# Kernel optimization log

Hardware: AMD Instinct MI355X
Metric: run time of the kernel (lower is better)

The kernel has to match this reference:

```python
import jax, jax.numpy as jnp
import numpy as np
import math

FACTOR = 5


def setup_inputs() -> dict:
    key = jax.random.key(0)
    k1, k2, k3, k4 = jax.random.split(key, 4)
    B, L, H, D = 4, 2048, 8, 64
    sample_k = FACTOR * int(np.ceil(np.log(L)))  # 40
    queries = jax.random.normal(k1, (B, L, H, D), dtype=jnp.float32)
    keys = jax.random.normal(k2, (B, L, H, D), dtype=jnp.float32)
    values = jax.random.normal(k3, (B, L, H, D), dtype=jnp.float32)
    # per-query sampled key indices (replaces the host-side random.sample loop)
    index_sample = jax.random.randint(k4, (L, sample_k), 0, L, dtype=jnp.int64)
    return {"queries": queries, "keys": keys, "values": values,
            "index_sample": index_sample}


def reference(queries, keys, values, index_sample):
    B, L_Q, H, D = queries.shape
    L_K = keys.shape[1]
    # [B, L, H, D] -> [B, H, L, D]
    Q = jnp.transpose(queries, (0, 2, 1, 3))
    K = jnp.transpose(keys, (0, 2, 1, 3))
    V = jnp.transpose(values, (0, 2, 1, 3))

    u = min(FACTOR * int(np.ceil(np.log(L_Q))), L_Q)  # n_top

    # --- _prob_QK: sample-score-topk-gather ---
    # K_sample[b,h,i,s,e] = K[b,h,index_sample[i,s],e]  -> [B,H,L_Q,S,E]
    K_sample = K[:, :, index_sample, :]
    Q_K_sample = jnp.einsum('bhie,bhise->bhis', Q, K_sample)  # [B,H,L_Q,S]
    M = Q_K_sample.max(axis=-1) - Q_K_sample.sum(axis=-1) / L_K  # [B,H,L_Q]
    _, M_top = jax.lax.top_k(M, u)  # [B,H,u] indices of sparse queries

    Q_reduce = jnp.take_along_axis(Q, M_top[..., None], axis=2)  # [B,H,u,D]
    scores = jnp.einsum('bhue,bhke->bhuk', Q_reduce, K)  # [B,H,u,L_K]

    scale = 1.0 / math.sqrt(D)
    scores = scores * scale

    # --- initial context (mask_flag=True): causal running sum of V ---
    context = jnp.cumsum(V, axis=2)  # [B,H,L_Q,D]

    # --- ProbMask: causal mask rows gathered at M_top ---
    causal_mask = jnp.arange(L_K)[None, None, None, :] > M_top[..., None]
    scores = jnp.where(causal_mask, -jnp.inf, scores)
    attn = jax.nn.softmax(scores, axis=-1)  # [B,H,u,L_K]

    update = jnp.einsum('bhuk,bhkd->bhud', attn, V)  # [B,H,u,D]
    bi = jnp.arange(B)[:, None, None]
    hi = jnp.arange(H)[None, :, None]
    context = context.at[bi, hi, M_top].set(update)

    # back to [B, L, H, D]
    return jnp.transpose(context, (0, 2, 1, 3))
```

## Files before the change

kernel.cpp:

```cpp
#include <hip/hip_runtime.h>
#include <hip/hip_bf16.h>
#include <math.h>


#define BB 4
#define LL 2048
#define HH 8
#define DD 64
#define SS 40
#define UU 40
#define CC 64
#define LC (LL/CC)

#define KC    64
#define NCH2  8
#define UG    2
#define KSUB  4
#define KPAD  68
#define PPAD  68

__global__ void k_measure(const float* __restrict__ Q, const float* __restrict__ K,
                          const int* __restrict__ idx, float* __restrict__ M)
{
    __shared__ float sMax[4][8];
    __shared__ float sSum[4][8];

    int t   = threadIdx.x;
    int blk = blockIdx.x;
    int b   = blk >> 11;
    int i   = blk & (LL - 1);
    int w    = t >> 6, lane = t & 63;
    int hg   = lane >> 4;
    int d4   = lane & 15;

    const int*   ip   = idx + (size_t)i * SS + w * 10;
    const float* Kb   = K + (size_t)b * (LL * HH * DD);
    const float* Qrow = Q + ((size_t)b * LL + i) * (HH * DD);

    float4 qa = *(const float4*)(Qrow + hg * DD + d4 * 4);
    float4 qb = *(const float4*)(Qrow + (4 + hg) * DD + d4 * 4);

    float maxa = -INFINITY, suma = 0.f;
    float maxb = -INFINITY, sumb = 0.f;

#define DOT4(q_, k_) (fmaf((q_).w, (k_).w, fmaf((q_).z, (k_).z, \
                      fmaf((q_).y, (k_).y, (q_).x * (k_).x))))

    float4 A0, B0, A1, B1;
    float4 A2, B2, A3, B3;
    {
        int k0 = ip[0], k1 = ip[1];
        const float* r0 = Kb + (size_t)k0 * (HH * DD);
        const float* r1 = Kb + (size_t)k1 * (HH * DD);
        A0 = *(const float4*)(r0 + hg * DD + d4 * 4);
        B0 = *(const float4*)(r0 + (4 + hg) * DD + d4 * 4);
        A1 = *(const float4*)(r1 + hg * DD + d4 * 4);
        B1 = *(const float4*)(r1 + (4 + hg) * DD + d4 * 4);
    }

    #pragma unroll
    for (int g = 0; g < 5; ++g) {
        if (g < 4) {
            int k2 = ip[2 * g + 2], k3 = ip[2 * g + 3];
            const float* r2 = Kb + (size_t)k2 * (HH * DD);
            const float* r3 = Kb + (size_t)k3 * (HH * DD);
            A2 = *(const float4*)(r2 + hg * DD + d4 * 4);
            B2 = *(const float4*)(r2 + (4 + hg) * DD + d4 * 4);
            A3 = *(const float4*)(r3 + hg * DD + d4 * 4);
            B3 = *(const float4*)(r3 + (4 + hg) * DD + d4 * 4);
        }
        __builtin_amdgcn_sched_barrier(0);

        float pa0 = DOT4(qa, A0), pb0 = DOT4(qb, B0);
        float pa1 = DOT4(qa, A1), pb1 = DOT4(qb, B1);
        #pragma unroll
        for (int off = 1; off < 16; off <<= 1) {
            pa0 += __shfl_xor(pa0, off);
            pb0 += __shfl_xor(pb0, off);
            pa1 += __shfl_xor(pa1, off);
            pb1 += __shfl_xor(pb1, off);
        }
        maxa = fmaxf(maxa, fmaxf(pa0, pa1));  suma += pa0 + pa1;
        maxb = fmaxf(maxb, fmaxf(pb0, pb1));  sumb += pb0 + pb1;

        A0 = A2; B0 = B2; A1 = A3; B1 = B3;
    }
#undef DOT4

    if (d4 == 0) {
        sMax[w][hg]     = maxa;  sSum[w][hg]     = suma;
        sMax[w][4 + hg] = maxb;  sSum[w][4 + hg] = sumb;
    }
    __syncthreads();

    if (t < 8) {
        float mx = sMax[0][t], sm = sSum[0][t];
        #pragma unroll
        for (int w2 = 1; w2 < 4; ++w2) {
            mx = fmaxf(mx, sMax[w2][t]);
            sm += sSum[w2][t];
        }
        M[((size_t)(b * HH + t)) * LL + i] = mx - sm * (1.0f / (float)LL);
    }
}

__global__ void k_topk(const float* __restrict__ M, int* __restrict__ topIdx)
{
    int lane = threadIdx.x;
    int bh   = blockIdx.x;
    const float* Mp = M + (size_t)bh * LL;

    unsigned k[32];
    #pragma unroll
    for (int r = 0; r < 32; ++r) {
        unsigned u = __float_as_uint(Mp[r * 64 + lane]);
        k[r] = (u & 0x80000000u) ? ~u : (u | 0x80000000u);
    }

    unsigned T = 0u;
    for (int bit = 31; bit >= 0; --bit) {
        unsigned cand = T | (1u << bit);
        int c = 0;
        #pragma unroll
        for (int r = 0; r < 32; ++r) c += (k[r] >= cand) ? 1 : 0;
        #pragma unroll
        for (int off = 1; off < 64; off <<= 1) c += __shfl_xor(c, off);
        if (c >= UU) T = cand;
    }

    int cGT = 0, cGE = 0;
    #pragma unroll
    for (int r = 0; r < 32; ++r) {
        cGT += (k[r] > T) ? 1 : 0;
        cGE += (k[r] >= T) ? 1 : 0;
    }
    #pragma unroll
    for (int off = 1; off < 64; off <<= 1) {
        cGT += __shfl_xor(cGT, off);
        cGE += __shfl_xor(cGE, off);
    }

    int need = UU - cGT;
    int X = LL;
    if (cGE - cGT != need) {
        int lo2 = 0;
        for (int bit = 10; bit >= 0; --bit) {
            int cand = lo2 | (1 << bit);
            int c = 0;
            #pragma unroll
            for (int r = 0; r < 32; ++r)
                c += (k[r] == T && (r * 64 + lane) < cand) ? 1 : 0;
            #pragma unroll
            for (int off = 1; off < 64; off <<= 1) c += __shfl_xor(c, off);
            if (c < need) lo2 = cand;
        }
        X = lo2 + 1;
    }

    unsigned inMask = 0u;
    int cnt = 0;
    #pragma unroll
    for (int r = 0; r < 32; ++r) {
        bool in = (k[r] > T) || (k[r] == T && (r * 64 + lane) < X);
        if (in) { inMask |= 1u << r; ++cnt; }
    }
    int pre = cnt;
    #pragma unroll
    for (int off = 1; off < 64; off <<= 1) {
        int v = __shfl_up(pre, off);
        if (lane >= off) pre += v;
    }
    int slot = pre - cnt;
    #pragma unroll
    for (int r = 0; r < 32; ++r) {
        if ((inMask >> r) & 1u) {
            topIdx[bh * UU + slot] = r * 64 + lane;
            ++slot;
        }
    }
}

__launch_bounds__(256, 2)
__global__ void k_attn(const float* __restrict__ Q, const float* __restrict__ K,
                       const float* __restrict__ V, const int* __restrict__ topIdx,
                       float* __restrict__ Oc, float* __restrict__ Lc)
{
    __shared__ float sK[2][KC][KPAD];
    __shared__ float sV[2][KC][KPAD];
    __shared__ float sP[20][PPAD];
    __shared__ int   sPos[UU];

    int t   = threadIdx.x;
    int bid = blockIdx.x;
    int bh  = bid / (NCH2 * UG);
    int rem = bid % (NCH2 * UG);
    int ch  = rem / UG, ug = rem % UG;
    int b   = bh / HH, h = bh % HH;

    if (t < UU) sPos[t] = topIdx[bh * UU + t];

    int j  = t & 63;
    int w  = t >> 6, lane = t & 63;
    int ub = __builtin_amdgcn_readfirstlane(w) * 5;

    int d4p = t & 15, tg = t >> 4;
    float4 a0 = {0,0,0,0}, a1 = {0,0,0,0};
    float den[5] = {0.f, 0.f, 0.f, 0.f, 0.f};

    const float* Kh = K + ((size_t)b * LL * HH + h) * DD;
    const float* Vh = V + ((size_t)b * LL * HH + h) * DD;

    float4 pk0, pk1, pk2, pk3, pv0, pv1, pv2, pv3;

#define ISSUE(k0_) { \
    size_t g0 = (size_t)((k0_) +  0 + tg) * (HH * DD) + d4p * 4; \
    size_t g1 = (size_t)((k0_) + 16 + tg) * (HH * DD) + d4p * 4; \
    size_t g2 = (size_t)((k0_) + 32 + tg) * (HH * DD) + d4p * 4; \
    size_t g3 = (size_t)((k0_) + 48 + tg) * (HH * DD) + d4p * 4; \
    pk0 = *(const float4*)(Kh + g0); pv0 = *(const float4*)(Vh + g0); \
    pk1 = *(const float4*)(Kh + g1); pv1 = *(const float4*)(Vh + g1); \
    pk2 = *(const float4*)(Kh + g2); pv2 = *(const float4*)(Vh + g2); \
    pk3 = *(const float4*)(Kh + g3); pv3 = *(const float4*)(Vh + g3); \
}
#define COMMIT(buf_) { \
    *(float4*)&sK[buf_][ 0 + tg][d4p * 4] = pk0; *(float4*)&sV[buf_][ 0 + tg][d4p * 4] = pv0; \
    *(float4*)&sK[buf_][16 + tg][d4p * 4] = pk1; *(float4*)&sV[buf_][16 + tg][d4p * 4] = pv1; \
    *(float4*)&sK[buf_][32 + tg][d4p * 4] = pk2; *(float4*)&sV[buf_][32 + tg][d4p * 4] = pv2; \
    *(float4*)&sK[buf_][48 + tg][d4p * 4] = pk3; *(float4*)&sV[buf_][48 + tg][d4p * 4] = pv3; \
}

    int k0base = ch * KSUB * KC;
    ISSUE(k0base);
    COMMIT(0);
    __syncthreads();

    #pragma unroll
    for (int sub = 0; sub < KSUB; ++sub) {
        int cur = sub & 1;
        int k0  = k0base + sub * KC;

        if (sub + 1 < KSUB) ISSUE(k0 + KC);

        int jg = k0 + j;
        {
            int p0 = __builtin_amdgcn_readfirstlane(sPos[ug * 20 + ub + 0]);
            int p1 = __builtin_amdgcn_readfirstlane(sPos[ug * 20 + ub + 1]);
            int p2 = __builtin_amdgcn_readfirstlane(sPos[ug * 20 + ub + 2]);
            int p3 = __builtin_amdgcn_readfirstlane(sPos[ug * 20 + ub + 3]);
            int p4 = __builtin_amdgcn_readfirstlane(sPos[ug * 20 + ub + 4]);
            const float* q0 = Q + (((size_t)b * LL + p0) * HH + h) * DD;
            const float* q1 = Q + (((size_t)b * LL + p1) * HH + h) * DD;
            const float* q2 = Q + (((size_t)b * LL + p2) * HH + h) * DD;
            const float* q3 = Q + (((size_t)b * LL + p3) * HH + h) * DD;
            const float* q4 = Q + (((size_t)b * LL + p4) * HH + h) * DD;
            float c0 = 0.f, c1 = 0.f, c2 = 0.f, c3 = 0.f, c4 = 0.f;
            #pragma unroll
            for (int d4 = 0; d4 < 16; ++d4) {
                float4 kk = *(const float4*)&sK[cur][j][d4 * 4];
                int d = d4 * 4;
                c0 = fmaf(kk.x, q0[d], c0); c0 = fmaf(kk.y, q0[d+1], c0);
                c0 = fmaf(kk.z, q0[d+2], c0); c0 = fmaf(kk.w, q0[d+3], c0);
                c1 = fmaf(kk.x, q1[d], c1); c1 = fmaf(kk.y, q1[d+1], c1);
                c1 = fmaf(kk.z, q1[d+2], c1); c1 = fmaf(kk.w, q1[d+3], c1);
                c2 = fmaf(kk.x, q2[d], c2); c2 = fmaf(kk.y, q2[d+1], c2);
                c2 = fmaf(kk.z, q2[d+2], c2); c2 = fmaf(kk.w, q2[d+3], c2);
                c3 = fmaf(kk.x, q3[d], c3); c3 = fmaf(kk.y, q3[d+1], c3);
                c3 = fmaf(kk.z, q3[d+2], c3); c3 = fmaf(kk.w, q3[d+3], c3);
                c4 = fmaf(kk.x, q4[d], c4); c4 = fmaf(kk.y, q4[d+1], c4);
                c4 = fmaf(kk.z, q4[d+2], c4); c4 = fmaf(kk.w, q4[d+3], c4);
            }
            float e0 = (jg > p0) ? 0.f : __expf(c0 * 0.125f);
            float e1 = (jg > p1) ? 0.f : __expf(c1 * 0.125f);
            float e2 = (jg > p2) ? 0.f : __expf(c2 * 0.125f);
            float e3 = (jg > p3) ? 0.f : __expf(c3 * 0.125f);
            float e4 = (jg > p4) ? 0.f : __expf(c4 * 0.125f);
            sP[ub + 0][j] = e0;
            sP[ub + 1][j] = e1;
            sP[ub + 2][j] = e2;
            sP[ub + 3][j] = e3;
            sP[ub + 4][j] = e4;
            #pragma unroll
            for (int off = 1; off < 64; off <<= 1) {
                e0 += __shfl_xor(e0, off);
                e1 += __shfl_xor(e1, off);
                e2 += __shfl_xor(e2, off);
                e3 += __shfl_xor(e3, off);
                e4 += __shfl_xor(e4, off);
            }
            den[0] += e0; den[1] += e1; den[2] += e2; den[3] += e3; den[4] += e4;
        }
        __syncthreads();

        if (sub + 1 < KSUB) {
            if (cur == 0) { COMMIT(1); } else { COMMIT(0); }
        }

        #pragma unroll 4
        for (int j4 = 0; j4 < KC / 4; ++j4) {
            float4 pj0 = *(const float4*)&sP[tg][j4 * 4];
            float4 pj1 = (tg < 4) ? *(const float4*)&sP[16 + tg][j4 * 4]
                                  : (float4){0,0,0,0};
            float4 va = *(const float4*)&sV[cur][j4 * 4 + 0][d4p * 4];
            float4 vb = *(const float4*)&sV[cur][j4 * 4 + 1][d4p * 4];
            float4 vc = *(const float4*)&sV[cur][j4 * 4 + 2][d4p * 4];
            float4 vd = *(const float4*)&sV[cur][j4 * 4 + 3][d4p * 4];
            a0.x = fmaf(pj0.x, va.x, fmaf(pj0.y, vb.x, fmaf(pj0.z, vc.x, fmaf(pj0.w, vd.x, a0.x))));
            a0.y = fmaf(pj0.x, va.y, fmaf(pj0.y, vb.y, fmaf(pj0.z, vc.y, fmaf(pj0.w, vd.y, a0.y))));
            a0.z = fmaf(pj0.x, va.z, fmaf(pj0.y, vb.z, fmaf(pj0.z, vc.z, fmaf(pj0.w, vd.z, a0.z))));
            a0.w = fmaf(pj0.x, va.w, fmaf(pj0.y, vb.w, fmaf(pj0.z, vc.w, fmaf(pj0.w, vd.w, a0.w))));
            a1.x = fmaf(pj1.x, va.x, fmaf(pj1.y, vb.x, fmaf(pj1.z, vc.x, fmaf(pj1.w, vd.x, a1.x))));
            a1.y = fmaf(pj1.x, va.y, fmaf(pj1.y, vb.y, fmaf(pj1.z, vc.y, fmaf(pj1.w, vd.y, a1.y))));
            a1.z = fmaf(pj1.x, va.z, fmaf(pj1.y, vb.z, fmaf(pj1.z, vc.z, fmaf(pj1.w, vd.z, a1.z))));
            a1.w = fmaf(pj1.x, va.w, fmaf(pj1.y, vb.w, fmaf(pj1.z, vc.w, fmaf(pj1.w, vd.w, a1.w))));
        }
        __syncthreads();
    }
#undef ISSUE
#undef COMMIT

    if (lane == 0) {
        int base = (bh * NCH2 + ch) * UU + ug * 20 + ub;
        Lc[base + 0] = den[0]; Lc[base + 1] = den[1]; Lc[base + 2] = den[2];
        Lc[base + 3] = den[3]; Lc[base + 4] = den[4];
    }
    {
        int u0g = ug * 20 + tg;
        size_t o0 = ((size_t)(bh * NCH2 + ch) * UU + u0g) * DD + d4p * 4;
        *(float4*)(Oc + o0) = a0;
        if (tg < 4) {
            int u1g = ug * 20 + 16 + tg;
            size_t o1 = ((size_t)(bh * NCH2 + ch) * UU + u1g) * DD + d4p * 4;
            *(float4*)(Oc + o1) = a1;
        }
    }
}

__global__ void k_chunksum(const float* __restrict__ V, float* __restrict__ chunkSum)
{
    int t  = threadIdx.x;
    int c  = blockIdx.x % CC;
    int bh = blockIdx.x / CC;
    int b  = bh / HH; int h = bh - b * HH;
    int d4 = t & 15, rs = t >> 4;

    float4 acc = {0,0,0,0};
    int l0 = c * LC;
    for (int l = l0 + rs; l < l0 + LC; l += 4) {
        float4 v = *(const float4*)(V + (((size_t)b * LL + l) * HH + h) * DD + d4 * 4);
        acc.x += v.x; acc.y += v.y; acc.z += v.z; acc.w += v.w;
    }
    acc.x += __shfl_xor(acc.x, 16); acc.y += __shfl_xor(acc.y, 16);
    acc.z += __shfl_xor(acc.z, 16); acc.w += __shfl_xor(acc.w, 16);
    acc.x += __shfl_xor(acc.x, 32); acc.y += __shfl_xor(acc.y, 32);
    acc.z += __shfl_xor(acc.z, 32); acc.w += __shfl_xor(acc.w, 32);
    if (t < 16)
        *(float4*)(chunkSum + ((size_t)bh * CC + c) * DD + d4 * 4) = acc;
}

__global__ void k_cumsum(const float* __restrict__ V, const float* __restrict__ chunkSum,
                         const float* __restrict__ Oc, const float* __restrict__ Lc,
                         const int* __restrict__ topIdx, float* __restrict__ out)
{
    int t  = threadIdx.x;
    int c  = blockIdx.x & (CC - 1);
    int bh = blockIdx.x >> 6;
    int b  = bh / HH; int h = bh - b * HH;
    int d4 = t & 15, s = t >> 4;

    const float4* CS4 = (const float4*)chunkSum;
    float4 off = {0,0,0,0};
    for (int c2 = s; c2 < c; c2 += 4) {
        float4 x = CS4[((size_t)bh * CC + c2) * 16 + d4];
        off.x += x.x; off.y += x.y; off.z += x.z; off.w += x.w;
    }
    off.x += __shfl_xor(off.x, 16); off.y += __shfl_xor(off.y, 16);
    off.z += __shfl_xor(off.z, 16); off.w += __shfl_xor(off.w, 16);
    off.x += __shfl_xor(off.x, 32); off.y += __shfl_xor(off.y, 32);
    off.z += __shfl_xor(off.z, 32); off.w += __shfl_xor(off.w, 32);

    int l0 = c * LC + s * 8;
    size_t base = (((size_t)b * LL + l0) * HH + h) * DD + d4 * 4;
    const size_t stride = (size_t)HH * DD;

    float4 v[8];
    #pragma unroll
    for (int r = 0; r < 8; ++r)
        v[r] = *(const float4*)(V + base + (size_t)r * stride);
    #pragma unroll
    for (int r = 1; r < 8; ++r) {
        v[r].x += v[r-1].x; v[r].y += v[r-1].y;
        v[r].z += v[r-1].z; v[r].w += v[r-1].w;
    }

    float4 inc = v[7];
    float4 p1;
    p1.x = __shfl_up(inc.x, 16); p1.y = __shfl_up(inc.y, 16);
    p1.z = __shfl_up(inc.z, 16); p1.w = __shfl_up(inc.w, 16);
    if (s >= 1) { inc.x += p1.x; inc.y += p1.y; inc.z += p1.z; inc.w += p1.w; }
    float4 p2;
    p2.x = __shfl_up(inc.x, 32); p2.y = __shfl_up(inc.y, 32);
    p2.z = __shfl_up(inc.z, 32); p2.w = __shfl_up(inc.w, 32);
    if (s >= 2) { inc.x += p2.x; inc.y += p2.y; inc.z += p2.z; inc.w += p2.w; }

    float4 add;
    add.x = off.x + inc.x - v[7].x;
    add.y = off.y + inc.y - v[7].y;
    add.z = off.z + inc.z - v[7].z;
    add.w = off.w + inc.w - v[7].w;

    #pragma unroll
    for (int r = 0; r < 8; ++r) {
        float4 o;
        o.x = v[r].x + add.x; o.y = v[r].y + add.y;
        o.z = v[r].z + add.z; o.w = v[r].w + add.w;
        *(float4*)(out + base + (size_t)r * stride) = o;
    }

    int l0c = c * LC;
    int anyTop = 0;
    #pragma unroll
    for (int u = 0; u < UU; ++u) {
        int pos = topIdx[bh * UU + u];
        anyTop |= (pos >= l0c && pos < l0c + LC) ? 1 : 0;
    }
    if (anyTop) {
        asm volatile("s_waitcnt vmcnt(0)" ::: "memory");
        for (int u = 0; u < UU; ++u) {
            int pos = topIdx[bh * UU + u];
            if (pos >= l0c && pos < l0c + LC) {
                float num = 0.f, den = 0.f;
                #pragma unroll
                for (int cc = 0; cc < NCH2; ++cc) {
                    num += Oc[((size_t)(bh * NCH2 + cc) * UU + u) * DD + t];
                    den += Lc[(bh * NCH2 + cc) * UU + u];
                }
                out[(((size_t)b * LL + pos) * HH + h) * DD + t] = num / den;
            }
        }
    }
}

extern "C" void kernel_launch(void* const* d_in, const int* in_sizes, int n_in,
                              void* d_out, int out_size, void* d_ws, size_t ws_size,
                              hipStream_t stream)
{
    const float* Q   = (const float*)d_in[0];
    const float* K   = (const float*)d_in[1];
    const float* V   = (const float*)d_in[2];
    const int*   idx = (const int*)d_in[3];
    float* out = (float*)d_out;

    float* M        = (float*)d_ws;
    int*   topIdx   = (int*)(M + (size_t)BB * HH * LL);
    float* Oc       = (float*)(topIdx + BB * HH * UU);
    float* Lc       = Oc + (size_t)BB * HH * NCH2 * UU * DD;
    float* chunkSum = Lc + BB * HH * NCH2 * UU;

    k_measure <<<BB * LL,             256, 0, stream>>>(Q, K, idx, M);
    k_topk    <<<BB * HH,              64, 0, stream>>>(M, topIdx);
    k_attn    <<<BB * HH * NCH2 * UG, 256, 0, stream>>>(Q, K, V, topIdx, Oc, Lc);
    k_chunksum<<<BB * HH * CC,         64, 0, stream>>>(V, chunkSum);
    k_cumsum  <<<BB * HH * CC,         64, 0, stream>>>(V, chunkSum, Oc, Lc, topIdx, out);
}
```

Measured before the change: 185.5 us.

## Merge independent stages into shared launches and add a separate finalize kernel

Folds the V chunk-sum into the measure kernel as extra blocks, and the causal cumsum into the top-k kernel as extra blocks. The top-u row overwrite moves into a small finalize kernel that runs after attention. The launch order changes so the cumsum no longer waits on attention and the cumsum path drops its per-chunk scan of topIdx. This cuts launch count and lets small independent work run alongside the larger stages, at the cost of heterogeneous blocks and a launch_bounds hint on the measure kernel.

```diff
diff --git a/kernel.cpp b/kernel.cpp
--- a/kernel.cpp
+++ b/kernel.cpp
@@ -19,14 +19,44 @@
 #define KPAD  68
 #define PPAD  68
 
-__global__ void k_measure(const float* __restrict__ Q, const float* __restrict__ K,
-                          const int* __restrict__ idx, float* __restrict__ M)
+#define NCSB  512
+#define NMSB  (BB*LL)
+#define NTKB  32
+#define NCUB  512
+
+__launch_bounds__(256, 8)
+__global__ void k_measure_cs(const float* __restrict__ Q, const float* __restrict__ K,
+                             const float* __restrict__ V, const int* __restrict__ idx,
+                             float* __restrict__ M, float* __restrict__ chunkSum)
 {
     __shared__ float sMax[4][8];
     __shared__ float sSum[4][8];
 
-    int t   = threadIdx.x;
-    int blk = blockIdx.x;
+    int t = threadIdx.x;
+
+    if (blockIdx.x < NCSB) {
+        int w = t >> 6, lane = t & 63;
+        int cI = blockIdx.x * 4 + w;
+        int bh = cI >> 6, c = cI & (CC - 1);
+        int b  = bh >> 3, h = bh & 7;
+        int d4 = lane & 15, rs = lane >> 4;
+
+        float4 acc = {0,0,0,0};
+        int l0 = c * LC;
+        for (int l = l0 + rs; l < l0 + LC; l += 4) {
+            float4 v = *(const float4*)(V + (((size_t)b * LL + l) * HH + h) * DD + d4 * 4);
+            acc.x += v.x; acc.y += v.y; acc.z += v.z; acc.w += v.w;
+        }
+        acc.x += __shfl_xor(acc.x, 16); acc.y += __shfl_xor(acc.y, 16);
+        acc.z += __shfl_xor(acc.z, 16); acc.w += __shfl_xor(acc.w, 16);
+        acc.x += __shfl_xor(acc.x, 32); acc.y += __shfl_xor(acc.y, 32);
+        acc.z += __shfl_xor(acc.z, 32); acc.w += __shfl_xor(acc.w, 32);
+        if (lane < 16)
+            *(float4*)(chunkSum + ((size_t)bh * CC + c) * DD + d4 * 4) = acc;
+        return;
+    }
+
+    int blk = blockIdx.x - NCSB;
     int b   = blk >> 11;
     int i   = blk & (LL - 1);
     int w    = t >> 6, lane = t & 63;
@@ -104,79 +134,142 @@
     }
 }
 
-__global__ void k_topk(const float* __restrict__ M, int* __restrict__ topIdx)
+__global__ void k_topk_cum(const float* __restrict__ M, int* __restrict__ topIdx,
+                           const float* __restrict__ V, const float* __restrict__ chunkSum,
+                           float* __restrict__ out)
 {
-    int lane = threadIdx.x;
-    int bh   = blockIdx.x;
-    const float* Mp = M + (size_t)bh * LL;
-
-    unsigned k[32];
-    #pragma unroll
-    for (int r = 0; r < 32; ++r) {
-        unsigned u = __float_as_uint(Mp[r * 64 + lane]);
-        k[r] = (u & 0x80000000u) ? ~u : (u | 0x80000000u);
-    }
-
-    unsigned T = 0u;
-    for (int bit = 31; bit >= 0; --bit) {
-        unsigned cand = T | (1u << bit);
-        int c = 0;
-        #pragma unroll
-        for (int r = 0; r < 32; ++r) c += (k[r] >= cand) ? 1 : 0;
-        #pragma unroll
-        for (int off = 1; off < 64; off <<= 1) c += __shfl_xor(c, off);
-        if (c >= UU) T = cand;
-    }
-
-    int cGT = 0, cGE = 0;
-    #pragma unroll
-    for (int r = 0; r < 32; ++r) {
-        cGT += (k[r] > T) ? 1 : 0;
-        cGE += (k[r] >= T) ? 1 : 0;
-    }
-    #pragma unroll
-    for (int off = 1; off < 64; off <<= 1) {
-        cGT += __shfl_xor(cGT, off);
-        cGE += __shfl_xor(cGE, off);
-    }
-
-    int need = UU - cGT;
-    int X = LL;
-    if (cGE - cGT != need) {
-        int lo2 = 0;
-        for (int bit = 10; bit >= 0; --bit) {
-            int cand = lo2 | (1 << bit);
+    if (blockIdx.x < NTKB) {
+        if (threadIdx.x >= 64) return;
+        int lane = threadIdx.x;
+        int bh   = blockIdx.x;
+        const float* Mp = M + (size_t)bh * LL;
+
+        unsigned k[32];
+        #pragma unroll
+        for (int r = 0; r < 32; ++r) {
+            unsigned u = __float_as_uint(Mp[r * 64 + lane]);
+            k[r] = (u & 0x80000000u) ? ~u : (u | 0x80000000u);
+        }
+
+        unsigned T = 0u;
+        for (int bit = 31; bit >= 0; --bit) {
+            unsigned cand = T | (1u << bit);
             int c = 0;
             #pragma unroll
-            for (int r = 0; r < 32; ++r)
-                c += (k[r] == T && (r * 64 + lane) < cand) ? 1 : 0;
+            for (int r = 0; r < 32; ++r) c += (k[r] >= cand) ? 1 : 0;
             #pragma unroll
             for (int off = 1; off < 64; off <<= 1) c += __shfl_xor(c, off);
-            if (c < need) lo2 = cand;
-        }
-        X = lo2 + 1;
-    }
-
-    unsigned inMask = 0u;
-    int cnt = 0;
+            if (c >= UU) T = cand;
+        }
+
+        int cGT = 0, cGE = 0;
+        #pragma unroll
+        for (int r = 0; r < 32; ++r) {
+            cGT += (k[r] > T) ? 1 : 0;
+            cGE += (k[r] >= T) ? 1 : 0;
+        }
+        #pragma unroll
+        for (int off = 1; off < 64; off <<= 1) {
+            cGT += __shfl_xor(cGT, off);
+            cGE += __shfl_xor(cGE, off);
+        }
+
+        int need = UU - cGT;
+        int X = LL;
+        if (cGE - cGT != need) {
+            int lo2 = 0;
+            for (int bit = 10; bit >= 0; --bit) {
+                int cand = lo2 | (1 << bit);
+                int c = 0;
+                #pragma unroll
+                for (int r = 0; r < 32; ++r)
+                    c += (k[r] == T && (r * 64 + lane) < cand) ? 1 : 0;
+                #pragma unroll
+                for (int off = 1; off < 64; off <<= 1) c += __shfl_xor(c, off);
+                if (c < need) lo2 = cand;
+            }
+            X = lo2 + 1;
+        }
+
+        unsigned inMask = 0u;
+        int cnt = 0;
+        #pragma unroll
+        for (int r = 0; r < 32; ++r) {
+            bool in = (k[r] > T) || (k[r] == T && (r * 64 + lane) < X);
+            if (in) { inMask |= 1u << r; ++cnt; }
+        }
+        int pre = cnt;
+        #pragma unroll
+        for (int off = 1; off < 64; off <<= 1) {
+            int v = __shfl_up(pre, off);
+            if (lane >= off) pre += v;
+        }
+        int slot = pre - cnt;
+        #pragma unroll
+        for (int r = 0; r < 32; ++r) {
+            if ((inMask >> r) & 1u) {
+                topIdx[bh * UU + slot] = r * 64 + lane;
+                ++slot;
+            }
+        }
+        return;
+    }
+
+    int t    = threadIdx.x;
+    int w    = t >> 6, lane = t & 63;
+    int cI   = (blockIdx.x - NTKB) * 4 + w;
+    int c    = cI & (CC - 1);
+    int bh   = cI >> 6;
+    int b    = bh >> 3, h = bh & 7;
+    int d4   = lane & 15, s = lane >> 4;
+
+    const float4* CS4 = (const float4*)chunkSum;
+    float4 off = {0,0,0,0};
+    for (int c2 = s; c2 < c; c2 += 4) {
+        float4 x = CS4[((size_t)bh * CC + c2) * 16 + d4];
+        off.x += x.x; off.y += x.y; off.z += x.z; off.w += x.w;
+    }
+    off.x += __shfl_xor(off.x, 16); off.y += __shfl_xor(off.y, 16);
+    off.z += __shfl_xor(off.z, 16); off.w += __shfl_xor(off.w, 16);
+    off.x += __shfl_xor(off.x, 32); off.y += __shfl_xor(off.y, 32);
+    off.z += __shfl_xor(off.z, 32); off.w += __shfl_xor(off.w, 32);
+
+    int l0 = c * LC + s * 8;
+    size_t base = (((size_t)b * LL + l0) * HH + h) * DD + d4 * 4;
+    const size_t stride = (size_t)HH * DD;
+
+    float4 v[8];
     #pragma unroll
-    for (int r = 0; r < 32; ++r) {
-        bool in = (k[r] > T) || (k[r] == T && (r * 64 + lane) < X);
-        if (in) { inMask |= 1u << r; ++cnt; }
-    }
-    int pre = cnt;
+    for (int r = 0; r < 8; ++r)
+        v[r] = *(const float4*)(V + base + (size_t)r * stride);
     #pragma unroll
-    for (int off = 1; off < 64; off <<= 1) {
-        int v = __shfl_up(pre, off);
-        if (lane >= off) pre += v;
-    }
-    int slot = pre - cnt;
+    for (int r = 1; r < 8; ++r) {
+        v[r].x += v[r-1].x; v[r].y += v[r-1].y;
+        v[r].z += v[r-1].z; v[r].w += v[r-1].w;
+    }
+
+    float4 inc = v[7];
+    float4 p1;
+    p1.x = __shfl_up(inc.x, 16); p1.y = __shfl_up(inc.y, 16);
+    p1.z = __shfl_up(inc.z, 16); p1.w = __shfl_up(inc.w, 16);
+    if (s >= 1) { inc.x += p1.x; inc.y += p1.y; inc.z += p1.z; inc.w += p1.w; }
+    float4 p2;
+    p2.x = __shfl_up(inc.x, 32); p2.y = __shfl_up(inc.y, 32);
+    p2.z = __shfl_up(inc.z, 32); p2.w = __shfl_up(inc.w, 32);
+    if (s >= 2) { inc.x += p2.x; inc.y += p2.y; inc.z += p2.z; inc.w += p2.w; }
+
+    float4 add;
+    add.x = off.x + inc.x - v[7].x;
+    add.y = off.y + inc.y - v[7].y;
+    add.z = off.z + inc.z - v[7].z;
+    add.w = off.w + inc.w - v[7].w;
+
     #pragma unroll
-    for (int r = 0; r < 32; ++r) {
-        if ((inMask >> r) & 1u) {
-            topIdx[bh * UU + slot] = r * 64 + lane;
-            ++slot;
-        }
+    for (int r = 0; r < 8; ++r) {
+        float4 o;
+        o.x = v[r].x + add.x; o.y = v[r].y + add.y;
+        o.z = v[r].z + add.z; o.w = v[r].w + add.w;
+        *(float4*)(out + base + (size_t)r * stride) = o;
     }
 }
 
@@ -335,108 +428,23 @@
     }
 }
 
-__global__ void k_chunksum(const float* __restrict__ V, float* __restrict__ chunkSum)
+__global__ void k_finalize(const float* __restrict__ Oc, const float* __restrict__ Lc,
+                           const int* __restrict__ topIdx, float* __restrict__ out)
 {
+    int bh = blockIdx.x;
+    int b  = bh / HH, h = bh % HH;
     int t  = threadIdx.x;
-    int c  = blockIdx.x % CC;
-    int bh = blockIdx.x / CC;
-    int b  = bh / HH; int h = bh - b * HH;
-    int d4 = t & 15, rs = t >> 4;
-
-    float4 acc = {0,0,0,0};
-    int l0 = c * LC;
-    for (int l = l0 + rs; l < l0 + LC; l += 4) {
-        float4 v = *(const float4*)(V + (((size_t)b * LL + l) * HH + h) * DD + d4 * 4);
-        acc.x += v.x; acc.y += v.y; acc.z += v.z; acc.w += v.w;
-    }
-    acc.x += __shfl_xor(acc.x, 16); acc.y += __shfl_xor(acc.y, 16);
-    acc.z += __shfl_xor(acc.z, 16); acc.w += __shfl_xor(acc.w, 16);
-    acc.x += __shfl_xor(acc.x, 32); acc.y += __shfl_xor(acc.y, 32);
-    acc.z += __shfl_xor(acc.z, 32); acc.w += __shfl_xor(acc.w, 32);
-    if (t < 16)
-        *(float4*)(chunkSum + ((size_t)bh * CC + c) * DD + d4 * 4) = acc;
-}
-
-__global__ void k_cumsum(const float* __restrict__ V, const float* __restrict__ chunkSum,
-                         const float* __restrict__ Oc, const float* __restrict__ Lc,
-                         const int* __restrict__ topIdx, float* __restrict__ out)
-{
-    int t  = threadIdx.x;
-    int c  = blockIdx.x & (CC - 1);
-    int bh = blockIdx.x >> 6;
-    int b  = bh / HH; int h = bh - b * HH;
-    int d4 = t & 15, s = t >> 4;
-
-    const float4* CS4 = (const float4*)chunkSum;
-    float4 off = {0,0,0,0};
-    for (int c2 = s; c2 < c; c2 += 4) {
-        float4 x = CS4[((size_t)bh * CC + c2) * 16 + d4];
-        off.x += x.x; off.y += x.y; off.z += x.z; off.w += x.w;
-    }
-    off.x += __shfl_xor(off.x, 16); off.y += __shfl_xor(off.y, 16);
-    off.z += __shfl_xor(off.z, 16); off.w += __shfl_xor(off.w, 16);
-    off.x += __shfl_xor(off.x, 32); off.y += __shfl_xor(off.y, 32);
-    off.z += __shfl_xor(off.z, 32); off.w += __shfl_xor(off.w, 32);
-
-    int l0 = c * LC + s * 8;
-    size_t base = (((size_t)b * LL + l0) * HH + h) * DD + d4 * 4;
-    const size_t stride = (size_t)HH * DD;
-
-    float4 v[8];
-    #pragma unroll
-    for (int r = 0; r < 8; ++r)
-        v[r] = *(const float4*)(V + base + (size_t)r * stride);
-    #pragma unroll
-    for (int r = 1; r < 8; ++r) {
-        v[r].x += v[r-1].x; v[r].y += v[r-1].y;
-        v[r].z += v[r-1].z; v[r].w += v[r-1].w;
-    }
-
-    float4 inc = v[7];
-    float4 p1;
-    p1.x = __shfl_up(inc.x, 16); p1.y = __shfl_up(inc.y, 16);
-    p1.z = __shfl_up(inc.z, 16); p1.w = __shfl_up(inc.w, 16);
-    if (s >= 1) { inc.x += p1.x; inc.y += p1.y; inc.z += p1.z; inc.w += p1.w; }
-    float4 p2;
-    p2.x = __shfl_up(inc.x, 32); p2.y = __shfl_up(inc.y, 32);
-    p2.z = __shfl_up(inc.z, 32); p2.w = __shfl_up(inc.w, 32);
-    if (s >= 2) { inc.x += p2.x; inc.y += p2.y; inc.z += p2.z; inc.w += p2.w; }
-
-    float4 add;
-    add.x = off.x + inc.x - v[7].x;
-    add.y = off.y + inc.y - v[7].y;
-    add.z = off.z + inc.z - v[7].z;
-    add.w = off.w + inc.w - v[7].w;
-
-    #pragma unroll
-    for (int r = 0; r < 8; ++r) {
-        float4 o;
-        o.x = v[r].x + add.x; o.y = v[r].y + add.y;
-        o.z = v[r].z + add.z; o.w = v[r].w + add.w;
-        *(float4*)(out + base + (size_t)r * stride) = o;
-    }
-
-    int l0c = c * LC;
-    int anyTop = 0;
-    #pragma unroll
-    for (int u = 0; u < UU; ++u) {
+    int d  = t & 63, w = t >> 6;
+    for (int i = 0; i < 10; ++i) {
+        int u = w * 10 + i;
         int pos = topIdx[bh * UU + u];
-        anyTop |= (pos >= l0c && pos < l0c + LC) ? 1 : 0;
-    }
-    if (anyTop) {
-        asm volatile("s_waitcnt vmcnt(0)" ::: "memory");
-        for (int u = 0; u < UU; ++u) {
-            int pos = topIdx[bh * UU + u];
-            if (pos >= l0c && pos < l0c + LC) {
-                float num = 0.f, den = 0.f;
-                #pragma unroll
-                for (int cc = 0; cc < NCH2; ++cc) {
-                    num += Oc[((size_t)(bh * NCH2 + cc) * UU + u) * DD + t];
-                    den += Lc[(bh * NCH2 + cc) * UU + u];
-                }
-                out[(((size_t)b * LL + pos) * HH + h) * DD + t] = num / den;
-            }
-        }
+        float num = 0.f, den = 0.f;
+        #pragma unroll
+        for (int c = 0; c < NCH2; ++c) {
+            num += Oc[((size_t)(bh * NCH2 + c) * UU + u) * DD + d];
+            den += Lc[(bh * NCH2 + c) * UU + u];
+        }
+        out[(((size_t)b * LL + pos) * HH + h) * DD + d] = num / den;
     }
 }
 
@@ -456,9 +464,8 @@
     float* Lc       = Oc + (size_t)BB * HH * NCH2 * UU * DD;
     float* chunkSum = Lc + BB * HH * NCH2 * UU;
 
-    k_measure <<<BB * LL,             256, 0, stream>>>(Q, K, idx, M);
-    k_topk    <<<BB * HH,              64, 0, stream>>>(M, topIdx);
-    k_attn    <<<BB * HH * NCH2 * UG, 256, 0, stream>>>(Q, K, V, topIdx, Oc, Lc);
-    k_chunksum<<<BB * HH * CC,         64, 0, stream>>>(V, chunkSum);
-    k_cumsum  <<<BB * HH * CC,         64, 0, stream>>>(V, chunkSum, Oc, Lc, topIdx, out);
-}
+    k_measure_cs<<<NCSB + NMSB,        256, 0, stream>>>(Q, K, V, idx, M, chunkSum);
+    k_topk_cum  <<<NTKB + NCUB,        256, 0, stream>>>(M, topIdx, V, chunkSum, out);
+    k_attn      <<<BB * HH * NCH2 * UG, 256, 0, stream>>>(Q, K, V, topIdx, Oc, Lc);
+    k_finalize  <<<BB * HH,            256, 0, stream>>>(Oc, Lc, topIdx, out);
+}
```

Measured after the change: 215.2 us. 16.0% more time.
